# Optimization experiments

Hardware: AMD Instinct MI355X
Metric: run time of the kernel (lower is better)

## Reference

```python
import jax, jax.numpy as jnp
import numpy as np

NUM_HEADS = 12
HEAD_DIM = 64
MASKED_BIAS = -10000.0


def setup_inputs() -> dict:
    key = jax.random.key(0)
    k1, k2, k3 = jax.random.split(key, 3)
    B, S, D = 2, 2048, 768
    return {
        "hidden_states": jax.random.normal(k1, (B, S, D), dtype=jnp.float32),
        "c_attn_w": jax.random.normal(k2, (D, 3 * D), dtype=jnp.float32) * 0.02,
        "c_attn_b": jnp.zeros((3 * D,), dtype=jnp.float32),
        "c_proj_w": jax.random.normal(k3, (D, D), dtype=jnp.float32) * 0.02,
        "c_proj_b": jnp.zeros((D,), dtype=jnp.float32),
    }


def _split_heads(x, B, S):
    # [B,S,D] -> [B,H,S,hd]
    return x.reshape(B, S, NUM_HEADS, HEAD_DIM).transpose(0, 2, 1, 3)


def reference(hidden_states, c_attn_w, c_attn_b, c_proj_w, c_proj_b):
    B, S, D = hidden_states.shape
    qkv = hidden_states @ c_attn_w + c_attn_b  # [B,S,3D]
    q, k, v = jnp.split(qkv, 3, axis=-1)
    q = _split_heads(q, B, S)
    k = _split_heads(k, B, S)
    v = _split_heads(v, B, S)

    # Unfused attention: full [B,H,S,S] scores, where-based causal mask
    attn_weights = jnp.einsum("bhqd,bhkd->bhqk", q, k)
    attn_weights = attn_weights / jnp.float32(HEAD_DIM) ** 0.5
    causal_mask = jnp.tril(jnp.ones((S, S), dtype=bool))[None, None]
    attn_weights = jnp.where(causal_mask, attn_weights,
                             jnp.asarray(MASKED_BIAS, attn_weights.dtype))
    attn_weights = jax.nn.softmax(attn_weights, axis=-1)
    attn_output = jnp.einsum("bhqk,bhkd->bhqd", attn_weights, v)

    # merge heads [B,H,S,hd] -> [B,S,D]
    attn_output = attn_output.transpose(0, 2, 1, 3).reshape(B, S, D)
    attn_output = attn_output @ c_proj_w + c_proj_b
    return attn_output
```

## Files before the change

### kernel.cpp

```cpp
#include <hip/hip_runtime.h>
#include <stdint.h>


constexpr int B_  = 2;
constexpr int S_  = 2048;
constexpr int D_  = 768;
constexpr int N3D = 3 * D_;
constexpr int M_  = B_ * S_;
constexpr int NTILE = 32 * 24;
#define QSCALE 0.1803368801111f
#define FIXED_M 8.0f

typedef __bf16 bv8 __attribute__((ext_vector_type(8)));
typedef float  fv4 __attribute__((ext_vector_type(4)));
typedef unsigned short uv4 __attribute__((ext_vector_type(4)));
typedef unsigned short uv8 __attribute__((ext_vector_type(8)));

__device__ inline unsigned short f2bf(float x) {
    __bf16 b = (__bf16)x;
    return __builtin_bit_cast(unsigned short, b);
}

__device__ inline fv4 mfma16(bv8 a, bv8 b, fv4 c) {
    return __builtin_amdgcn_mfma_f32_16x16x32_bf16(a, b, c, 0, 0, 0);
}

#define GLOAD_LDS16(g, l)                                                        \
    __builtin_amdgcn_global_load_lds(                                            \
        (__attribute__((address_space(1))) void*)(g),                            \
        (__attribute__((address_space(3))) void*)(l), 16, 0, 0)

#define VMCNT4() asm volatile("s_waitcnt vmcnt(4)" ::: "memory")
#define VMCNT0() asm volatile("s_waitcnt vmcnt(0)" ::: "memory")
#define BAR()                                                                    \
    do { asm volatile("" ::: "memory"); __builtin_amdgcn_s_barrier();            \
         asm volatile("" ::: "memory"); } while (0)

__global__ __launch_bounds__(256)
void prep(const float* __restrict__ hs, const float* __restrict__ wqkv,
          const float* __restrict__ wproj, unsigned short* __restrict__ hsb,
          unsigned short* __restrict__ wqkvT, unsigned short* __restrict__ wprojT,
          int* __restrict__ cnt)
{
    __shared__ float tl[32][33];
    const int bid = blockIdx.x, t = threadIdx.x;
    if (bid == 0 && t < 4) cnt[t] = 0;

    if (bid < 1536) {
        const size_t i = ((size_t)bid * 256 + t) * 8;
        const float4 a = *(const float4*)&hs[i];
        const float4 b = *(const float4*)&hs[i + 4];
        uv8 o;
        o[0] = f2bf(a.x); o[1] = f2bf(a.y); o[2] = f2bf(a.z); o[3] = f2bf(a.w);
        o[4] = f2bf(b.x); o[5] = f2bf(b.y); o[6] = f2bf(b.z); o[7] = f2bf(b.w);
        *(uv8*)&hsb[i] = o;
        return;
    }

    const float* W;
    unsigned short* WT;
    int K, N, bx, by;
    if (bid < 3264) {
        W = wqkv; WT = wqkvT; K = 768; N = 2304;
        const int b2 = bid - 1536; bx = b2 % 72; by = b2 / 72;
    } else {
        W = wproj; WT = wprojT; K = 768; N = 768;
        const int b2 = bid - 3264; bx = b2 % 24; by = b2 / 24;
    }
    const int n0 = bx * 32, k0 = by * 32;
    {
        const int r = t >> 3, c = (t & 7) * 4;
        const float4 v = *(const float4*)&W[(size_t)(k0 + r) * N + n0 + c];
        tl[r][c + 0] = v.x; tl[r][c + 1] = v.y; tl[r][c + 2] = v.z; tl[r][c + 3] = v.w;
    }
    __syncthreads();
    {
        const int rn = t >> 3, ck = (t & 7) * 4;
        uv4 o;
        o[0] = f2bf(tl[ck + 0][rn]); o[1] = f2bf(tl[ck + 1][rn]);
        o[2] = f2bf(tl[ck + 2][rn]); o[3] = f2bf(tl[ck + 3][rn]);
        *(uv4*)&WT[(size_t)(n0 + rn) * K + k0 + ck] = o;
    }
}

template<bool QKV>
__global__ __launch_bounds__(256)
void gemm_bf16(const unsigned short* __restrict__ A, const unsigned short* __restrict__ BT,
               const float* __restrict__ bias, float* __restrict__ Cf,
               unsigned short* __restrict__ Qb, unsigned short* __restrict__ Kb,
               unsigned short* __restrict__ VTb, int M, int N, int K, int gx)
{
    __shared__ unsigned short smem[24576];
    unsigned short* const sA0 = smem;
    unsigned short* const sB0 = smem + 12288;

    const int t = threadIdx.x, w = t >> 6, lane = t & 63;
    const int l15 = lane & 15, l4 = lane >> 4;
    const int nwg = gridDim.x, cpx = nwg >> 3;
    const int orig = blockIdx.x;
    const int swz = (orig & 7) * cpx + (orig >> 3);
    const int m0 = (swz / gx) * 128, n0 = (swz % gx) * 128;
    const int wr = w >> 1, wc = w & 1;

    fv4 acc[4][4];
#pragma unroll
    for (int i = 0; i < 4; ++i)
#pragma unroll
        for (int j = 0; j < 4; ++j) acc[i][j] = fv4{0.f, 0.f, 0.f, 0.f};

    const int r0 = w * 16 + (lane >> 2);
    const int c0 = (lane & 3) ^ ((r0 >> 1) & 3);
    const int r1 = (w + 4) * 16 + (lane >> 2);
    const int c1 = (lane & 3) ^ ((r1 >> 1) & 3);

    auto stage = [&](int buf, int k0) {
        GLOAD_LDS16(A  + (size_t)(m0 + r0) * K + k0 + c0 * 8, sA0 + buf * 4096 + w * 512);
        GLOAD_LDS16(A  + (size_t)(m0 + r1) * K + k0 + c1 * 8, sA0 + buf * 4096 + (w + 4) * 512);
        GLOAD_LDS16(BT + (size_t)(n0 + r0) * K + k0 + c0 * 8, sB0 + buf * 4096 + w * 512);
        GLOAD_LDS16(BT + (size_t)(n0 + r1) * K + k0 + c1 * 8, sB0 + buf * 4096 + (w + 4) * 512);
    };

    stage(0, 0);
    stage(1, 32);
    const int nt = K >> 5;
    for (int tt = 0; tt < nt; ++tt) {
        if (tt + 1 < nt) VMCNT4(); else VMCNT0();
        BAR();
        if (tt + 2 < nt) stage((tt + 2) % 3, (tt + 2) * 32);
        const int cur = tt % 3;

        bv8 af[4], bf[4];
#pragma unroll
        for (int i = 0; i < 4; ++i) {
            const int r = wr * 64 + i * 16 + l15;
            const int c = l4 ^ ((r >> 1) & 3);
            af[i] = *(const bv8*)&sA0[cur * 4096 + r * 32 + c * 8];
        }
#pragma unroll
        for (int j = 0; j < 4; ++j) {
            const int r = wc * 64 + j * 16 + l15;
            const int c = l4 ^ ((r >> 1) & 3);
            bf[j] = *(const bv8*)&sB0[cur * 4096 + r * 32 + c * 8];
        }
        __builtin_amdgcn_s_setprio(1);
#pragma unroll
        for (int i = 0; i < 4; ++i)
#pragma unroll
            for (int j = 0; j < 4; ++j)
                acc[i][j] = mfma16(af[i], bf[j], acc[i][j]);
        __builtin_amdgcn_s_setprio(0);
    }

    if (QKV) {
        const int sect = n0 / 768;
        const int rem0 = n0 - sect * 768;
        if (sect < 2) {
            __syncthreads();
            const float qs = (sect == 0) ? QSCALE : 1.0f;
#pragma unroll
            for (int jf = 0; jf < 4; ++jf) {
                const int c = wc * 64 + jf * 16 + l15;
                const float bb = bias[n0 + c];
                const int ch = c >> 3, off = c & 7;
#pragma unroll
                for (int i = 0; i < 4; ++i) {
                    const int rb = wr * 64 + i * 16 + l4 * 4;
#pragma unroll
                    for (int reg = 0; reg < 4; ++reg) {
                        const int r = rb + reg;
                        smem[r * 128 + ((ch ^ (r & 15)) << 3) + off] =
                            f2bf((acc[i][jf][reg] + bb) * qs);
                    }
                }
            }
            __syncthreads();
            unsigned short* const dstQK = (sect == 0) ? Qb : Kb;
            const int brow = m0 >> 11, sbase = m0 & 2047, hb = rem0 >> 6;
#pragma unroll
            for (int u = 0; u < 8; ++u) {
                const int ID = t + 256 * u;
                const int s = ID >> 4, ch = ID & 15;
                const int hh = ch >> 3, dc = ch & 7;
                const uv8 v = *(const uv8*)&smem[s * 128 + ((ch ^ (s & 15)) << 3)];
                const size_t bh = (size_t)brow * 12 + hb + hh;
                *(uv8*)&dstQK[(bh * 2048 + sbase + s) * 64 + dc * 8] = v;
            }
        } else {
#pragma unroll
            for (int jf = 0; jf < 4; ++jf) {
                const int col = n0 + wc * 64 + jf * 16 + l15;
                const float bb = bias[col];
                const int rem = col - 2 * 768;
                const int hh_ = rem >> 6, d = rem & 63;
#pragma unroll
                for (int i = 0; i < 4; ++i) {
                    const int rowb = m0 + wr * 64 + i * 16 + l4 * 4;
                    const size_t bh = (size_t)(rowb >> 11) * 12 + hh_;
                    const int s0 = rowb & 2047;
                    uv4 pk;
#pragma unroll
                    for (int reg = 0; reg < 4; ++reg) pk[reg] = f2bf(acc[i][jf][reg] + bb);
                    *(uv4*)&VTb[(bh * 64 + d) * 2048 + s0] = pk;
                }
            }
        }
    } else {
#pragma unroll
        for (int jf = 0; jf < 4; ++jf) {
            const int col = n0 + wc * 64 + jf * 16 + l15;
            const float bb = bias[col];
#pragma unroll
            for (int i = 0; i < 4; ++i) {
                const int rowb = m0 + wr * 64 + i * 16 + l4 * 4;
#pragma unroll
                for (int reg = 0; reg < 4; ++reg)
                    Cf[(size_t)(rowb + reg) * N + col] = acc[i][jf][reg] + bb;
            }
        }
    }
}

__global__ __launch_bounds__(256)
void flash_mfma(const unsigned short* __restrict__ Qb, const unsigned short* __restrict__ Kb,
                const unsigned short* __restrict__ VTb, unsigned short* __restrict__ outb,
                int* __restrict__ cnt)
{
    __shared__ unsigned short sK [3][64 * 64];
    __shared__ unsigned short sVT[3][64 * 64];
    __shared__ unsigned short sP [4][16 * 64];
    __shared__ int sj;

    const int t = threadIdx.x, w = t >> 6, lane = t & 63;
    const int l15 = lane & 15, l4 = lane >> 4;

    const int sr0 = w * 8 + (lane >> 3), sc0 = (lane & 7) ^ (sr0 & 7);
    const int sr1 = (w + 4) * 8 + (lane >> 3), sc1 = (lane & 7) ^ (sr1 & 7);

    for (;;) {
        if (t == 0) sj = atomicAdd(cnt, 1);
        __syncthreads();
        const int j = sj;
        if (j >= NTILE) return;
        const int qt = 31 - j / 24;
        const int bh = j - (j / 24) * 24;
        const int b = bh / 12, h = bh - b * 12;
        const int qrow = qt * 64 + w * 16;

        const unsigned short* Kbase = Kb  + (size_t)bh * 2048 * 64;
        const unsigned short* Vbase = VTb + (size_t)bh * 64 * 2048;

        auto stage = [&](int buf, int kt) {
            GLOAD_LDS16(Kbase + (size_t)(kt * 64 + sr0) * 64 + sc0 * 8, &sK[buf][w * 512]);
            GLOAD_LDS16(Kbase + (size_t)(kt * 64 + sr1) * 64 + sc1 * 8, &sK[buf][(w + 4) * 512]);
            GLOAD_LDS16(Vbase + (size_t)sr0 * 2048 + kt * 64 + sc0 * 8, &sVT[buf][w * 512]);
            GLOAD_LDS16(Vbase + (size_t)sr1 * 2048 + kt * 64 + sc1 * 8, &sVT[buf][(w + 4) * 512]);
        };

        bv8 qf[2];
        {
            const unsigned short* qp = Qb + ((size_t)bh * 2048 + qrow + l15) * 64 + l4 * 8;
            qf[0] = *(const bv8*)qp;
            qf[1] = *(const bv8*)(qp + 32);
        }

        fv4 o[4];
#pragma unroll
        for (int jf = 0; jf < 4; ++jf) o[jf] = fv4{0.f, 0.f, 0.f, 0.f};
        float l_ = 0.f;

        stage(0, 0);
        if (qt >= 1) stage(1, 1);

        for (int kt = 0; kt <= qt; ++kt) {
            if (kt < qt) VMCNT4(); else VMCNT0();
            BAR();
            if (kt + 2 <= qt) stage((kt + 2) % 3, kt + 2);
            const int cur = kt % 3;

            fv4 st[4];
            __builtin_amdgcn_s_setprio(1);
#pragma unroll
            for (int jf = 0; jf < 4; ++jf) {
                st[jf] = fv4{-FIXED_M, -FIXED_M, -FIXED_M, -FIXED_M};
                const int kr = jf * 16 + l15;
#pragma unroll
                for (int hh = 0; hh < 2; ++hh) {
                    const bv8 ka = *(const bv8*)&sK[cur][kr * 64 + (((hh * 4 + l4) ^ (kr & 7)) * 8)];
                    st[jf] = mfma16(ka, qf[hh], st[jf]);
                }
            }
            __builtin_amdgcn_s_setprio(0);

            float ps[16];
            const int qg = qrow + l15;
            if (kt == qt) {
#pragma unroll
                for (int jf = 0; jf < 4; ++jf)
#pragma unroll
                    for (int reg = 0; reg < 4; ++reg) {
                        const int kvg = kt * 64 + jf * 16 + l4 * 4 + reg;
                        ps[jf * 4 + reg] = (kvg > qg) ? -30000.f : st[jf][reg];
                    }
            } else {
#pragma unroll
                for (int jf = 0; jf < 4; ++jf)
#pragma unroll
                    for (int reg = 0; reg < 4; ++reg) ps[jf * 4 + reg] = st[jf][reg];
            }
            float la0 = 0.f, la1 = 0.f, la2 = 0.f, la3 = 0.f;
#pragma unroll
            for (int u = 0; u < 16; u += 4) {
                const float p0 = exp2f(ps[u + 0]); ps[u + 0] = p0; la0 += p0;
                const float p1 = exp2f(ps[u + 1]); ps[u + 1] = p1; la1 += p1;
                const float p2 = exp2f(ps[u + 2]); ps[u + 2] = p2; la2 += p2;
                const float p3 = exp2f(ps[u + 3]); ps[u + 3] = p3; la3 += p3;
            }
            l_ += (la0 + la1) + (la2 + la3);

#pragma unroll
            for (int jf = 0; jf < 4; ++jf) {
                uv4 pk;
#pragma unroll
                for (int reg = 0; reg < 4; ++reg) pk[reg] = f2bf(ps[jf * 4 + reg]);
                const int chunk = jf * 2 + (l4 >> 1);
                *(uv4*)&sP[w][l15 * 64 + ((chunk ^ (l15 & 7)) * 8) + (l4 & 1) * 4] = pk;
            }

            bv8 pa[2];
#pragma unroll
            for (int hh = 0; hh < 2; ++hh)
                pa[hh] = *(const bv8*)&sP[w][l15 * 64 + (((hh * 4 + l4) ^ (l15 & 7)) * 8)];
            __builtin_amdgcn_s_setprio(1);
#pragma unroll
            for (int jf = 0; jf < 4; ++jf) {
                const int dr = jf * 16 + l15;
#pragma unroll
                for (int hh = 0; hh < 2; ++hh) {
                    const bv8 vb = *(const bv8*)&sVT[cur][dr * 64 + (((hh * 4 + l4) ^ (dr & 7)) * 8)];
                    o[jf] = mfma16(pa[hh], vb, o[jf]);
                }
            }
            __builtin_amdgcn_s_setprio(0);
        }

        l_ += __shfl_xor(l_, 16);
        l_ += __shfl_xor(l_, 32);
        const float inv = 1.0f / l_;
        float invq[4];
#pragma unroll
        for (int reg = 0; reg < 4; ++reg) invq[reg] = __shfl(inv, l4 * 4 + reg);
#pragma unroll
        for (int jf = 0; jf < 4; ++jf)
#pragma unroll
            for (int reg = 0; reg < 4; ++reg)
                outb[(size_t)(b * S_ + qrow + l4 * 4 + reg) * D_ + h * 64 + jf * 16 + l15] =
                    f2bf(o[jf][reg] * invq[reg]);
    }
}

extern "C" void kernel_launch(void* const* d_in, const int* in_sizes, int n_in,
                              void* d_out, int out_size, void* d_ws, size_t ws_size,
                              hipStream_t stream)
{
    const float* hs    = (const float*)d_in[0];
    const float* wqkv  = (const float*)d_in[1];
    const float* bqkv  = (const float*)d_in[2];
    const float* wproj = (const float*)d_in[3];
    const float* bproj = (const float*)d_in[4];
    float* out = (float*)d_out;

    unsigned short* hsb    = (unsigned short*)d_ws;
    unsigned short* wqkvT  = hsb    + (size_t)M_ * D_;
    unsigned short* wprojT = wqkvT  + (size_t)N3D * D_;
    unsigned short* Qb     = wprojT + (size_t)D_ * D_;
    unsigned short* Kb     = Qb     + (size_t)24 * 2048 * 64;
    unsigned short* VTb    = Kb     + (size_t)24 * 2048 * 64;
    unsigned short* attnb  = VTb    + (size_t)24 * 2048 * 64;
    int* cnt = (int*)(attnb + (size_t)M_ * D_);

    prep<<<3840, 256, 0, stream>>>(hs, wqkv, wproj, hsb, wqkvT, wprojT, cnt);
    gemm_bf16<true><<<(N3D / 128) * (M_ / 128), 256, 0, stream>>>(
        hsb, wqkvT, bqkv, nullptr, Qb, Kb, VTb, M_, N3D, D_, N3D / 128);
    flash_mfma<<<512, 256, 0, stream>>>(Qb, Kb, VTb, attnb, cnt);
    gemm_bf16<false><<<(D_ / 128) * (M_ / 128), 256, 0, stream>>>(
        attnb, wprojT, bproj, out, nullptr, nullptr, nullptr, M_, D_, D_, D_ / 128);
}
```

Baseline: 163.8 us.

## Specialize QKV GEMM, add 64x64-tile projection GEMM, double-buffer flash loads

The templated GEMM is split into a QKV-specialized kernel with compile-time sizes, hoisted load pointers and an LDS-staged transposed V store that writes coalesced 16-byte rows. The output projection moves to a new 64x64-tile GEMM with 768 blocks so more workgroups are available to fill the GPU. The flash attention kernel drops from triple to double buffering with incremented pointers, which cuts LDS use but waits on all outstanding loads every iteration. Several unrelated changes are bundled here, and the shallower prefetch pipelines could expose more memory latency.

```diff
diff --git a/kernel.cpp b/kernel.cpp
--- a/kernel.cpp
+++ b/kernel.cpp
@@ -83,23 +83,22 @@
     }
 }
 
-template<bool QKV>
 __global__ __launch_bounds__(256)
-void gemm_bf16(const unsigned short* __restrict__ A, const unsigned short* __restrict__ BT,
-               const float* __restrict__ bias, float* __restrict__ Cf,
-               unsigned short* __restrict__ Qb, unsigned short* __restrict__ Kb,
-               unsigned short* __restrict__ VTb, int M, int N, int K, int gx)
+void gemm_qkv(const unsigned short* __restrict__ A, const unsigned short* __restrict__ BT,
+              const float* __restrict__ bias,
+              unsigned short* __restrict__ Qb, unsigned short* __restrict__ Kb,
+              unsigned short* __restrict__ VTb)
 {
     __shared__ unsigned short smem[24576];
     unsigned short* const sA0 = smem;
     unsigned short* const sB0 = smem + 12288;
+    constexpr int K = 768, NT = 24;
 
     const int t = threadIdx.x, w = t >> 6, lane = t & 63;
     const int l15 = lane & 15, l4 = lane >> 4;
-    const int nwg = gridDim.x, cpx = nwg >> 3;
     const int orig = blockIdx.x;
-    const int swz = (orig & 7) * cpx + (orig >> 3);
-    const int m0 = (swz / gx) * 128, n0 = (swz % gx) * 128;
+    const int swz = (orig & 7) * 72 + (orig >> 3);
+    const int m0 = (swz / 18) * 128, n0 = (swz % 18) * 128;
     const int wr = w >> 1, wc = w & 1;
 
     fv4 acc[4][4];
@@ -113,21 +112,25 @@
     const int r1 = (w + 4) * 16 + (lane >> 2);
     const int c1 = (lane & 3) ^ ((r1 >> 1) & 3);
 
+    const unsigned short* ap0 = A  + (size_t)(m0 + r0) * K + c0 * 8;
+    const unsigned short* ap1 = A  + (size_t)(m0 + r1) * K + c1 * 8;
+    const unsigned short* bp0 = BT + (size_t)(n0 + r0) * K + c0 * 8;
+    const unsigned short* bp1 = BT + (size_t)(n0 + r1) * K + c1 * 8;
+
     auto stage = [&](int buf, int k0) {
-        GLOAD_LDS16(A  + (size_t)(m0 + r0) * K + k0 + c0 * 8, sA0 + buf * 4096 + w * 512);
-        GLOAD_LDS16(A  + (size_t)(m0 + r1) * K + k0 + c1 * 8, sA0 + buf * 4096 + (w + 4) * 512);
-        GLOAD_LDS16(BT + (size_t)(n0 + r0) * K + k0 + c0 * 8, sB0 + buf * 4096 + w * 512);
-        GLOAD_LDS16(BT + (size_t)(n0 + r1) * K + k0 + c1 * 8, sB0 + buf * 4096 + (w + 4) * 512);
+        GLOAD_LDS16(ap0 + k0, sA0 + buf * 4096 + w * 512);
+        GLOAD_LDS16(ap1 + k0, sA0 + buf * 4096 + (w + 4) * 512);
+        GLOAD_LDS16(bp0 + k0, sB0 + buf * 4096 + w * 512);
+        GLOAD_LDS16(bp1 + k0, sB0 + buf * 4096 + (w + 4) * 512);
     };
 
     stage(0, 0);
     stage(1, 32);
-    const int nt = K >> 5;
-    for (int tt = 0; tt < nt; ++tt) {
-        if (tt + 1 < nt) VMCNT4(); else VMCNT0();
+    int cur = 0, s2 = 2;
+    for (int tt = 0; tt < NT; ++tt) {
+        if (tt + 1 < NT) VMCNT4(); else VMCNT0();
         BAR();
-        if (tt + 2 < nt) stage((tt + 2) % 3, (tt + 2) * 32);
-        const int cur = tt % 3;
+        if (tt + 2 < NT) { stage(s2, (tt + 2) * 32); s2 = (s2 == 2) ? 0 : s2 + 1; }
 
         bv8 af[4], bf[4];
 #pragma unroll
@@ -149,73 +152,143 @@
             for (int j = 0; j < 4; ++j)
                 acc[i][j] = mfma16(af[i], bf[j], acc[i][j]);
         __builtin_amdgcn_s_setprio(0);
-    }
-
-    if (QKV) {
-        const int sect = n0 / 768;
-        const int rem0 = n0 - sect * 768;
-        if (sect < 2) {
-            __syncthreads();
-            const float qs = (sect == 0) ? QSCALE : 1.0f;
-#pragma unroll
-            for (int jf = 0; jf < 4; ++jf) {
-                const int c = wc * 64 + jf * 16 + l15;
-                const float bb = bias[n0 + c];
-                const int ch = c >> 3, off = c & 7;
-#pragma unroll
-                for (int i = 0; i < 4; ++i) {
-                    const int rb = wr * 64 + i * 16 + l4 * 4;
-#pragma unroll
-                    for (int reg = 0; reg < 4; ++reg) {
-                        const int r = rb + reg;
-                        smem[r * 128 + ((ch ^ (r & 15)) << 3) + off] =
-                            f2bf((acc[i][jf][reg] + bb) * qs);
-                    }
+        cur = (cur == 2) ? 0 : cur + 1;
+    }
+
+    const int sect = n0 / 768;
+    const int rem0 = n0 - sect * 768;
+    const int brow = m0 >> 11, sbase = m0 & 2047, hb = rem0 >> 6;
+    __syncthreads();
+
+    if (sect < 2) {
+        const float qs = (sect == 0) ? QSCALE : 1.0f;
+#pragma unroll
+        for (int jf = 0; jf < 4; ++jf) {
+            const int c = wc * 64 + jf * 16 + l15;
+            const float bb = bias[n0 + c];
+            const int ch = c >> 3, off = c & 7;
+#pragma unroll
+            for (int i = 0; i < 4; ++i) {
+                const int rb = wr * 64 + i * 16 + l4 * 4;
+#pragma unroll
+                for (int reg = 0; reg < 4; ++reg) {
+                    const int r = rb + reg;
+                    smem[r * 128 + ((ch ^ (r & 15)) << 3) + off] =
+                        f2bf((acc[i][jf][reg] + bb) * qs);
                 }
             }
-            __syncthreads();
-            unsigned short* const dstQK = (sect == 0) ? Qb : Kb;
-            const int brow = m0 >> 11, sbase = m0 & 2047, hb = rem0 >> 6;
-#pragma unroll
-            for (int u = 0; u < 8; ++u) {
-                const int ID = t + 256 * u;
-                const int s = ID >> 4, ch = ID & 15;
-                const int hh = ch >> 3, dc = ch & 7;
-                const uv8 v = *(const uv8*)&smem[s * 128 + ((ch ^ (s & 15)) << 3)];
-                const size_t bh = (size_t)brow * 12 + hb + hh;
-                *(uv8*)&dstQK[(bh * 2048 + sbase + s) * 64 + dc * 8] = v;
-            }
-        } else {
-#pragma unroll
-            for (int jf = 0; jf < 4; ++jf) {
-                const int col = n0 + wc * 64 + jf * 16 + l15;
-                const float bb = bias[col];
-                const int rem = col - 2 * 768;
-                const int hh_ = rem >> 6, d = rem & 63;
-#pragma unroll
-                for (int i = 0; i < 4; ++i) {
-                    const int rowb = m0 + wr * 64 + i * 16 + l4 * 4;
-                    const size_t bh = (size_t)(rowb >> 11) * 12 + hh_;
-                    const int s0 = rowb & 2047;
-                    uv4 pk;
-#pragma unroll
-                    for (int reg = 0; reg < 4; ++reg) pk[reg] = f2bf(acc[i][jf][reg] + bb);
-                    *(uv4*)&VTb[(bh * 64 + d) * 2048 + s0] = pk;
-                }
-            }
+        }
+        __syncthreads();
+        unsigned short* const dstQK = (sect == 0) ? Qb : Kb;
+#pragma unroll
+        for (int u = 0; u < 8; ++u) {
+            const int ID = t + 256 * u;
+            const int s = ID >> 4, ch = ID & 15;
+            const int hh = ch >> 3, dc = ch & 7;
+            const uv8 v = *(const uv8*)&smem[s * 128 + ((ch ^ (s & 15)) << 3)];
+            const size_t bh = (size_t)brow * 12 + hb + hh;
+            *(uv8*)&dstQK[(bh * 2048 + sbase + s) * 64 + dc * 8] = v;
         }
     } else {
 #pragma unroll
         for (int jf = 0; jf < 4; ++jf) {
-            const int col = n0 + wc * 64 + jf * 16 + l15;
-            const float bb = bias[col];
+            const int d2 = wc * 64 + jf * 16 + l15;
+            const float bb = bias[n0 + d2];
+            const int dmask = d2 & 31;
 #pragma unroll
             for (int i = 0; i < 4; ++i) {
-                const int rowb = m0 + wr * 64 + i * 16 + l4 * 4;
-#pragma unroll
-                for (int reg = 0; reg < 4; ++reg)
-                    Cf[(size_t)(rowb + reg) * N + col] = acc[i][jf][reg] + bb;
-            }
+                const int cs = wr * 16 + i * 4 + l4;
+                uv4 pk;
+#pragma unroll
+                for (int reg = 0; reg < 4; ++reg) pk[reg] = f2bf(acc[i][jf][reg] + bb);
+                *(uv4*)&smem[d2 * 128 + ((cs ^ dmask) << 2)] = pk;
+            }
+        }
+        __syncthreads();
+#pragma unroll
+        for (int u = 0; u < 8; ++u) {
+            const int ID = t + 256 * u;
+            const int rd = ID >> 4, cp = ID & 15;
+            const int k = rd & 31;
+            const uv4 a = *(const uv4*)&smem[rd * 128 + (((2 * cp) ^ k) << 2)];
+            const uv4 b2 = *(const uv4*)&smem[rd * 128 + (((2 * cp + 1) ^ k) << 2)];
+            uv8 v;
+            v[0] = a[0]; v[1] = a[1]; v[2] = a[2]; v[3] = a[3];
+            v[4] = b2[0]; v[5] = b2[1]; v[6] = b2[2]; v[7] = b2[3];
+            const size_t bh = (size_t)brow * 12 + hb + (rd >> 6);
+            *(uv8*)&VTb[(bh * 64 + (rd & 63)) * 2048 + sbase + cp * 8] = v;
+        }
+    }
+}
+
+__global__ __launch_bounds__(256)
+void gemm64(const unsigned short* __restrict__ A, const unsigned short* __restrict__ BT,
+            const float* __restrict__ bias, float* __restrict__ Cf)
+{
+    __shared__ unsigned short sA[2][2048];
+    __shared__ unsigned short sB[2][2048];
+    constexpr int K = 768, NT = 24;
+
+    const int t = threadIdx.x, w = t >> 6, lane = t & 63;
+    const int l15 = lane & 15, l4 = lane >> 4;
+    const int orig = blockIdx.x;
+    const int swz = (orig & 7) * 96 + (orig >> 3);
+    const int m0 = (swz / 12) * 64, n0 = (swz % 12) * 64;
+    const int wr = w >> 1, wc = w & 1;
+
+    fv4 acc[2][2];
+#pragma unroll
+    for (int i = 0; i < 2; ++i)
+#pragma unroll
+        for (int j = 0; j < 2; ++j) acc[i][j] = fv4{0.f, 0.f, 0.f, 0.f};
+
+    const int r0 = w * 16 + (lane >> 2);
+    const int c0 = (lane & 3) ^ ((r0 >> 1) & 3);
+    const unsigned short* ap = A  + (size_t)(m0 + r0) * K + c0 * 8;
+    const unsigned short* bp = BT + (size_t)(n0 + r0) * K + c0 * 8;
+
+    GLOAD_LDS16(ap, sA[0] + w * 512);
+    GLOAD_LDS16(bp, sB[0] + w * 512);
+    for (int tt = 0; tt < NT; ++tt) {
+        const int cur = tt & 1;
+        VMCNT0();
+        BAR();
+        if (tt + 1 < NT) {
+            GLOAD_LDS16(ap + (tt + 1) * 32, sA[cur ^ 1] + w * 512);
+            GLOAD_LDS16(bp + (tt + 1) * 32, sB[cur ^ 1] + w * 512);
+        }
+        bv8 af[2], bf[2];
+#pragma unroll
+        for (int i = 0; i < 2; ++i) {
+            const int r = wr * 32 + i * 16 + l15;
+            const int c = l4 ^ ((r >> 1) & 3);
+            af[i] = *(const bv8*)&sA[cur][r * 32 + c * 8];
+        }
+#pragma unroll
+        for (int j = 0; j < 2; ++j) {
+            const int r = wc * 32 + j * 16 + l15;
+            const int c = l4 ^ ((r >> 1) & 3);
+            bf[j] = *(const bv8*)&sB[cur][r * 32 + c * 8];
+        }
+        __builtin_amdgcn_s_setprio(1);
+#pragma unroll
+        for (int i = 0; i < 2; ++i)
+#pragma unroll
+            for (int j = 0; j < 2; ++j)
+                acc[i][j] = mfma16(af[i], bf[j], acc[i][j]);
+        __builtin_amdgcn_s_setprio(0);
+    }
+
+#pragma unroll
+    for (int j = 0; j < 2; ++j) {
+        const int col = n0 + wc * 32 + j * 16 + l15;
+        const float bb = bias[col];
+#pragma unroll
+        for (int i = 0; i < 2; ++i) {
+            const int rowb = m0 + wr * 32 + i * 16 + l4 * 4;
+#pragma unroll
+            for (int reg = 0; reg < 4; ++reg)
+                Cf[(size_t)(rowb + reg) * 768 + col] = acc[i][j][reg] + bb;
         }
     }
 }
@@ -225,9 +298,9 @@
                 const unsigned short* __restrict__ VTb, unsigned short* __restrict__ outb,
                 int* __restrict__ cnt)
 {
-    __shared__ unsigned short sK [3][64 * 64];
-    __shared__ unsigned short sVT[3][64 * 64];
-    __shared__ unsigned short sP [4][16 * 64];
+    __shared__ unsigned short sK [2][4096];
+    __shared__ unsigned short sVT[2][4096];
+    __shared__ unsigned short sP [4][1024];
     __shared__ int sj;
 
     const int t = threadIdx.x, w = t >> 6, lane = t & 63;
@@ -246,15 +319,10 @@
         const int b = bh / 12, h = bh - b * 12;
         const int qrow = qt * 64 + w * 16;
 
-        const unsigned short* Kbase = Kb  + (size_t)bh * 2048 * 64;
-        const unsigned short* Vbase = VTb + (size_t)bh * 64 * 2048;
-
-        auto stage = [&](int buf, int kt) {
-            GLOAD_LDS16(Kbase + (size_t)(kt * 64 + sr0) * 64 + sc0 * 8, &sK[buf][w * 512]);
-            GLOAD_LDS16(Kbase + (size_t)(kt * 64 + sr1) * 64 + sc1 * 8, &sK[buf][(w + 4) * 512]);
-            GLOAD_LDS16(Vbase + (size_t)sr0 * 2048 + kt * 64 + sc0 * 8, &sVT[buf][w * 512]);
-            GLOAD_LDS16(Vbase + (size_t)sr1 * 2048 + kt * 64 + sc1 * 8, &sVT[buf][(w + 4) * 512]);
-        };
+        const unsigned short* kp0 = Kb  + (size_t)bh * 131072 + sr0 * 64 + sc0 * 8;
+        const unsigned short* kp1 = Kb  + (size_t)bh * 131072 + sr1 * 64 + sc1 * 8;
+        const unsigned short* vp0 = VTb + (size_t)bh * 131072 + sr0 * 2048 + sc0 * 8;
+        const unsigned short* vp1 = VTb + (size_t)bh * 131072 + sr1 * 2048 + sc1 * 8;
 
         bv8 qf[2];
         {
@@ -268,14 +336,23 @@
         for (int jf = 0; jf < 4; ++jf) o[jf] = fv4{0.f, 0.f, 0.f, 0.f};
         float l_ = 0.f;
 
-        stage(0, 0);
-        if (qt >= 1) stage(1, 1);
+        GLOAD_LDS16(kp0, &sK[0][w * 512]);
+        GLOAD_LDS16(kp1, &sK[0][(w + 4) * 512]);
+        GLOAD_LDS16(vp0, &sVT[0][w * 512]);
+        GLOAD_LDS16(vp1, &sVT[0][(w + 4) * 512]);
+        kp0 += 4096; kp1 += 4096; vp0 += 64; vp1 += 64;
 
         for (int kt = 0; kt <= qt; ++kt) {
-            if (kt < qt) VMCNT4(); else VMCNT0();
+            const int cur = kt & 1;
+            VMCNT0();
             BAR();
-            if (kt + 2 <= qt) stage((kt + 2) % 3, kt + 2);
-            const int cur = kt % 3;
+            if (kt < qt) {
+                GLOAD_LDS16(kp0, &sK[cur ^ 1][w * 512]);
+                GLOAD_LDS16(kp1, &sK[cur ^ 1][(w + 4) * 512]);
+                GLOAD_LDS16(vp0, &sVT[cur ^ 1][w * 512]);
+                GLOAD_LDS16(vp1, &sVT[cur ^ 1][(w + 4) * 512]);
+                kp0 += 4096; kp1 += 4096; vp0 += 64; vp1 += 64;
+            }
 
             fv4 st[4];
             __builtin_amdgcn_s_setprio(1);
@@ -379,9 +456,7 @@
     int* cnt = (int*)(attnb + (size_t)M_ * D_);
 
     prep<<<3840, 256, 0, stream>>>(hs, wqkv, wproj, hsb, wqkvT, wprojT, cnt);
-    gemm_bf16<true><<<(N3D / 128) * (M_ / 128), 256, 0, stream>>>(
-        hsb, wqkvT, bqkv, nullptr, Qb, Kb, VTb, M_, N3D, D_, N3D / 128);
+    gemm_qkv<<<576, 256, 0, stream>>>(hsb, wqkvT, bqkv, Qb, Kb, VTb);
     flash_mfma<<<512, 256, 0, stream>>>(Qb, Kb, VTb, attnb, cnt);
-    gemm_bf16<false><<<(D_ / 128) * (M_ / 128), 256, 0, stream>>>(
-        attnb, wprojT, bproj, out, nullptr, nullptr, nullptr, M_, D_, D_, D_ / 128);
-}
+    gemm64<<<768, 256, 0, stream>>>(attnb, wprojT, bproj, out);
+}
```

After: 164.7 us. About the same (+0.6%).
